# Kernel optimization log

Hardware: AMD Instinct MI355X
Metric: run time of the kernel (lower is better)

Reference implementation:

```python
import jax, jax.numpy as jnp
import numpy as np

VB = 1.0
N_COORD = 2
N_WALKERS = 2_000_000


def setup_inputs() -> dict:
    key = jax.random.key(0)
    Rs = jax.random.normal(key, (N_WALKERS, N_COORD, 3), dtype=jnp.float32)
    return {
        "Rs": Rs,
        "a": jnp.ones((1,), dtype=jnp.float32),
        "c100_re": jnp.ones((1,), dtype=jnp.float32),
        "c100_im": jnp.zeros((1,), dtype=jnp.float32),
        "c200_re": jnp.ones((1,), dtype=jnp.float32),
        "c200_im": jnp.zeros((1,), dtype=jnp.float32),
    }


def reference(Rs, a, c100_re, c100_im, c200_re, c200_im):
    # Rs: [N, 2, 3] walker coordinates for 2 particles.
    Z = 1.0 / a[0]
    r = jnp.sqrt(jnp.sum(Rs * Rs, axis=-1))            # [N, 2] radial coords
    Y00 = 1.0 / jnp.sqrt(4.0 * jnp.float32(np.pi))     # spherical harmonic Y_00

    # hydrogen-like s-orbitals: psi_100, psi_200 (per particle)
    psi100 = (2.0 * Z ** 1.5 * jnp.exp(-Z * r)) * Y00                       # [N, 2]
    psi200 = (Z ** 1.5 / (2.0 * jnp.sqrt(jnp.float32(2.0)))
              * (2.0 - Z * r) * jnp.exp(-0.5 * Z * r)) * Y00                # [N, 2]

    # product wavefunctions over the two coordinates
    Psi1 = jnp.prod(psi100, axis=-1)   # [N]
    Psi2 = jnp.prod(psi200, axis=-1)   # [N]

    # Laplacian of s-orbital product: sum_a (Z^2/n^2 - 2Z/r_a) * Psi
    inv_r = 1.0 / r
    lap1 = jnp.sum(Z * Z - 2.0 * Z * inv_r, axis=-1)          # [N], n=1
    lap2 = jnp.sum(0.25 * Z * Z - 2.0 * Z * inv_r, axis=-1)   # [N], n=2

    # pairwise Coulomb potential (single pair for N_coord=2)
    d12 = jnp.sqrt(jnp.sum((Rs[:, 0, :] - Rs[:, 1, :]) ** 2, axis=-1))  # [N]
    V = -VB / d12

    H1 = -0.5 * lap1 * Psi1 + V * Psi1   # [N]
    H2 = -0.5 * lap2 * Psi2 + V * Psi2   # [N]

    c1 = (c100_re[0] + 1j * c100_im[0]).astype(jnp.complex64)
    c2 = (c200_re[0] + 1j * c200_im[0]).astype(jnp.complex64)

    H_psi = c1 * H1 + c2 * H2                         # [N] complex64
    psi = c1 * Psi1 + c2 * Psi2                       # [N] complex64
    psistar = jnp.conj(c1) * Psi1 + jnp.conj(c2) * Psi2  # Psi1/Psi2 are real

    hammy = psistar * H_psi
    psi2 = psistar * psi
    return jnp.mean(hammy) / jnp.mean(psi2)
```

## Files before the change

### kernel.cpp

```cpp
#include <hip/hip_runtime.h>
#include <math.h>

#define BLOCK  256
#define GRID   1024
#define NCOMP  7

__device__ __forceinline__ void walker_accum(
    float x0, float y0, float z0, float x1, float y1, float z1,
    float Z, float zz, float ch, float K1, float K2,
    float& a11, float& a22, float& a12, float& a21,
    float& p11, float& p22, float& p12)
{
    float rr0 = x0*x0 + y0*y0 + z0*z0;
    float rr1 = x1*x1 + y1*y1 + z1*z1;
    float q0  = __builtin_amdgcn_rsqf(rr0);
    float q1  = __builtin_amdgcn_rsqf(rr1);
    float r0  = rr0 * q0;
    float r1  = rr1 * q1;

    float h0 = __builtin_amdgcn_exp2f(ch * r0);
    float h1 = __builtin_amdgcn_exp2f(ch * r1);
    float hh = h0 * h1;

    float Psi1 = K1 * (hh * hh);
    float Psi2 = K2 * (2.0f - Z*r0) * (2.0f - Z*r1) * hh;

    float sinv = q0 + q1;

    float dx = x0 - x1, dy = y0 - y1, dz = z0 - z1;
    float dd = dx*dx + dy*dy + dz*dz;
    float V  = -__builtin_amdgcn_rsqf(dd);

    float t1 = Z * sinv - zz + V;
    float t2 = Z * sinv - 0.25f * zz + V;
    float H1 = t1 * Psi1;
    float H2 = t2 * Psi2;

    a11 += Psi1 * H1;
    a22 += Psi2 * H2;
    a12 += Psi1 * H2;
    a21 += Psi2 * H1;
    p11 += Psi1 * Psi1;
    p22 += Psi2 * Psi2;
    p12 += Psi1 * Psi2;
}

__global__ __launch_bounds__(BLOCK) void wvfn_partial(
    const float4* __restrict__ Rs4,
    const float* __restrict__ a_p,
    double* __restrict__ partials,
    int npairs)
{
    const float Z  = 1.0f / a_p[0];
    const float zz = Z * Z;
    const float ch = -0.5f * Z * 1.4426950408889634f;
    const float Y00sq = 0.07957747154594767f;
    const float Z3 = Z * zz;
    const float K1 = 4.0f * Z3 * Y00sq;
    const float K2 = 0.125f * Z3 * Y00sq;

    float a11 = 0.f, a22 = 0.f, a12 = 0.f, a21 = 0.f;
    float p11 = 0.f, p22 = 0.f, p12 = 0.f;

    const int tid    = blockIdx.x * BLOCK + threadIdx.x;
    const int stride = GRID * BLOCK;
    for (int j = tid; j < npairs; j += stride) {
        float4 v0 = Rs4[3*j + 0];
        float4 v1 = Rs4[3*j + 1];
        float4 v2 = Rs4[3*j + 2];
        walker_accum(v0.x, v0.y, v0.z, v0.w, v1.x, v1.y,
                     Z, zz, ch, K1, K2, a11, a22, a12, a21, p11, p22, p12);
        walker_accum(v1.z, v1.w, v2.x, v2.y, v2.z, v2.w,
                     Z, zz, ch, K1, K2, a11, a22, a12, a21, p11, p22, p12);
    }

    double s[NCOMP] = { (double)a11, (double)a22, (double)a12, (double)a21,
                        (double)p11, (double)p22, (double)p12 };

    for (int off = 32; off > 0; off >>= 1) {
        #pragma unroll
        for (int c = 0; c < NCOMP; ++c) s[c] += __shfl_down(s[c], off);
    }

    __shared__ double sm[NCOMP][BLOCK / 64];
    int wid  = threadIdx.x >> 6;
    int lane = threadIdx.x & 63;
    if (lane == 0) {
        #pragma unroll
        for (int c = 0; c < NCOMP; ++c) sm[c][wid] = s[c];
    }
    __syncthreads();
    if (threadIdx.x == 0) {
        #pragma unroll
        for (int c = 0; c < NCOMP; ++c) {
            double t = 0.0;
            for (int w = 0; w < BLOCK / 64; ++w) t += sm[c][w];
            partials[c * GRID + blockIdx.x] = t;
        }
    }
}

__global__ __launch_bounds__(BLOCK) void wvfn_finish(
    const double* __restrict__ partials,
    const float* __restrict__ c1r_p, const float* __restrict__ c1i_p,
    const float* __restrict__ c2r_p, const float* __restrict__ c2i_p,
    float* __restrict__ out, int out_size)
{
    double s[NCOMP];
    #pragma unroll
    for (int c = 0; c < NCOMP; ++c) s[c] = 0.0;
    for (int b = threadIdx.x; b < GRID; b += BLOCK) {
        #pragma unroll
        for (int c = 0; c < NCOMP; ++c) s[c] += partials[c * GRID + b];
    }
    for (int off = 32; off > 0; off >>= 1) {
        #pragma unroll
        for (int c = 0; c < NCOMP; ++c) s[c] += __shfl_down(s[c], off);
    }
    __shared__ double sm[NCOMP][BLOCK / 64];
    int wid  = threadIdx.x >> 6;
    int lane = threadIdx.x & 63;
    if (lane == 0) {
        #pragma unroll
        for (int c = 0; c < NCOMP; ++c) sm[c][wid] = s[c];
    }
    __syncthreads();
    if (threadIdx.x == 0) {
        double A11 = 0, A22 = 0, A12 = 0, A21 = 0, P11 = 0, P22 = 0, P12 = 0;
        for (int w = 0; w < BLOCK / 64; ++w) {
            A11 += sm[0][w]; A22 += sm[1][w]; A12 += sm[2][w]; A21 += sm[3][w];
            P11 += sm[4][w]; P22 += sm[5][w]; P12 += sm[6][w];
        }
        double c1r = (double)c1r_p[0], c1i = (double)c1i_p[0];
        double c2r = (double)c2r_p[0], c2i = (double)c2i_p[0];
        double m1 = c1r*c1r + c1i*c1i;
        double m2 = c2r*c2r + c2i*c2i;
        double u  = c1r*c2r + c1i*c2i;
        double v  = c1r*c2i - c1i*c2r;

        double Hre = m1*A11 + m2*A22 + u*(A12 + A21);
        double Him = v*(A12 - A21);
        double Den = m1*P11 + m2*P22 + 2.0*u*P12;

        out[0] = (float)(Hre / Den);
        if (out_size > 1) out[1] = (float)(Him / Den);
    }
}

extern "C" void kernel_launch(void* const* d_in, const int* in_sizes, int n_in,
                              void* d_out, int out_size, void* d_ws, size_t ws_size,
                              hipStream_t stream) {
    const float4* Rs4 = (const float4*)d_in[0];
    const float* a_p  = (const float*)d_in[1];
    const float* c1r  = (const float*)d_in[2];
    const float* c1i  = (const float*)d_in[3];
    const float* c2r  = (const float*)d_in[4];
    const float* c2i  = (const float*)d_in[5];

    int N      = in_sizes[0] / 6;
    int npairs = N / 2;

    double* partials = (double*)d_ws;

    wvfn_partial<<<GRID, BLOCK, 0, stream>>>(Rs4, a_p, partials, npairs);
    wvfn_finish<<<1, BLOCK, 0, stream>>>(partials, c1r, c1i, c2r, c2i,
                                         (float*)d_out, out_size);
}
```

Before: 21.89 us.

## Double grid, unroll loop by two strides, use float block reductions

```diff
diff --git a/kernel.cpp b/kernel.cpp
--- a/kernel.cpp
+++ b/kernel.cpp
@@ -2,7 +2,7 @@
 #include <math.h>
 
 #define BLOCK  256
-#define GRID   1024
+#define GRID   2048
 #define NCOMP  7
 
 __device__ __forceinline__ void walker_accum(
@@ -48,7 +48,7 @@
 __global__ __launch_bounds__(BLOCK) void wvfn_partial(
     const float4* __restrict__ Rs4,
     const float* __restrict__ a_p,
-    double* __restrict__ partials,
+    float* __restrict__ partials,
     int npairs)
 {
     const float Z  = 1.0f / a_p[0];
@@ -64,7 +64,26 @@
 
     const int tid    = blockIdx.x * BLOCK + threadIdx.x;
     const int stride = GRID * BLOCK;
-    for (int j = tid; j < npairs; j += stride) {
+
+    int j = tid;
+    for (; j + stride < npairs; j += 2 * stride) {
+        int j2 = j + stride;
+        float4 v0 = Rs4[3*j  + 0];
+        float4 v1 = Rs4[3*j  + 1];
+        float4 v2 = Rs4[3*j  + 2];
+        float4 w0 = Rs4[3*j2 + 0];
+        float4 w1 = Rs4[3*j2 + 1];
+        float4 w2 = Rs4[3*j2 + 2];
+        walker_accum(v0.x, v0.y, v0.z, v0.w, v1.x, v1.y,
+                     Z, zz, ch, K1, K2, a11, a22, a12, a21, p11, p22, p12);
+        walker_accum(v1.z, v1.w, v2.x, v2.y, v2.z, v2.w,
+                     Z, zz, ch, K1, K2, a11, a22, a12, a21, p11, p22, p12);
+        walker_accum(w0.x, w0.y, w0.z, w0.w, w1.x, w1.y,
+                     Z, zz, ch, K1, K2, a11, a22, a12, a21, p11, p22, p12);
+        walker_accum(w1.z, w1.w, w2.x, w2.y, w2.z, w2.w,
+                     Z, zz, ch, K1, K2, a11, a22, a12, a21, p11, p22, p12);
+    }
+    if (j < npairs) {
         float4 v0 = Rs4[3*j + 0];
         float4 v1 = Rs4[3*j + 1];
         float4 v2 = Rs4[3*j + 2];
@@ -74,15 +93,14 @@
                      Z, zz, ch, K1, K2, a11, a22, a12, a21, p11, p22, p12);
     }
 
-    double s[NCOMP] = { (double)a11, (double)a22, (double)a12, (double)a21,
-                        (double)p11, (double)p22, (double)p12 };
+    float s[NCOMP] = { a11, a22, a12, a21, p11, p22, p12 };
 
     for (int off = 32; off > 0; off >>= 1) {
         #pragma unroll
         for (int c = 0; c < NCOMP; ++c) s[c] += __shfl_down(s[c], off);
     }
 
-    __shared__ double sm[NCOMP][BLOCK / 64];
+    __shared__ float sm[NCOMP][BLOCK / 64];
     int wid  = threadIdx.x >> 6;
     int lane = threadIdx.x & 63;
     if (lane == 0) {
@@ -93,7 +111,7 @@
     if (threadIdx.x == 0) {
         #pragma unroll
         for (int c = 0; c < NCOMP; ++c) {
-            double t = 0.0;
+            float t = 0.0f;
             for (int w = 0; w < BLOCK / 64; ++w) t += sm[c][w];
             partials[c * GRID + blockIdx.x] = t;
         }
@@ -101,28 +119,31 @@
 }
 
 __global__ __launch_bounds__(BLOCK) void wvfn_finish(
-    const double* __restrict__ partials,
+    const float4* __restrict__ partials4,
     const float* __restrict__ c1r_p, const float* __restrict__ c1i_p,
     const float* __restrict__ c2r_p, const float* __restrict__ c2i_p,
     float* __restrict__ out, int out_size)
 {
-    double s[NCOMP];
+    const int ROWV = GRID / 4;
+    double u[NCOMP];
     #pragma unroll
-    for (int c = 0; c < NCOMP; ++c) s[c] = 0.0;
-    for (int b = threadIdx.x; b < GRID; b += BLOCK) {
-        #pragma unroll
-        for (int c = 0; c < NCOMP; ++c) s[c] += partials[c * GRID + b];
+    for (int c = 0; c < NCOMP; ++c) u[c] = 0.0;
+
+    for (int i = threadIdx.x; i < NCOMP * ROWV; i += BLOCK) {
+        int c = i / ROWV;
+        float4 v = partials4[i];
+        u[c] += (double)((v.x + v.y) + (v.z + v.w));
     }
     for (int off = 32; off > 0; off >>= 1) {
         #pragma unroll
-        for (int c = 0; c < NCOMP; ++c) s[c] += __shfl_down(s[c], off);
+        for (int c = 0; c < NCOMP; ++c) u[c] += __shfl_down(u[c], off);
     }
     __shared__ double sm[NCOMP][BLOCK / 64];
     int wid  = threadIdx.x >> 6;
     int lane = threadIdx.x & 63;
     if (lane == 0) {
         #pragma unroll
-        for (int c = 0; c < NCOMP; ++c) sm[c][wid] = s[c];
+        for (int c = 0; c < NCOMP; ++c) sm[c][wid] = u[c];
     }
     __syncthreads();
     if (threadIdx.x == 0) {
@@ -135,12 +156,12 @@
         double c2r = (double)c2r_p[0], c2i = (double)c2i_p[0];
         double m1 = c1r*c1r + c1i*c1i;
         double m2 = c2r*c2r + c2i*c2i;
-        double u  = c1r*c2r + c1i*c2i;
-        double v  = c1r*c2i - c1i*c2r;
+        double uu = c1r*c2r + c1i*c2i;
+        double vv = c1r*c2i - c1i*c2r;
 
-        double Hre = m1*A11 + m2*A22 + u*(A12 + A21);
-        double Him = v*(A12 - A21);
-        double Den = m1*P11 + m2*P22 + 2.0*u*P12;
+        double Hre = m1*A11 + m2*A22 + uu*(A12 + A21);
+        double Him = vv*(A12 - A21);
+        double Den = m1*P11 + m2*P22 + 2.0*uu*P12;
 
         out[0] = (float)(Hre / Den);
         if (out_size > 1) out[1] = (float)(Him / Den);
@@ -160,9 +181,10 @@
     int N      = in_sizes[0] / 6;
     int npairs = N / 2;
 
-    double* partials = (double*)d_ws;
+    float* partials = (float*)d_ws;
 
     wvfn_partial<<<GRID, BLOCK, 0, stream>>>(Rs4, a_p, partials, npairs);
-    wvfn_finish<<<1, BLOCK, 0, stream>>>(partials, c1r, c1i, c2r, c2i,
+    wvfn_finish<<<1, BLOCK, 0, stream>>>((const float4*)partials,
+                                         c1r, c1i, c2r, c2i,
                                          (float*)d_out, out_size);
 }
```

Result: faster. 21.39 us (-2.3%).
